# Kernel optimization log

Measured on AMD Instinct MI355X. Metric: run time of the kernel, lower is better.

The kernel has to match this reference:

```python
import jax, jax.numpy as jnp
import numpy as np

NUM_BINS = 10
NUM_CLASSES = 128
ALPHA = 0.999
LABEL_SMOOTHING = 0.0


def setup_inputs() -> dict:
    key = jax.random.key(0)
    k1, k2, k3 = jax.random.split(key, 3)
    B, T, C = 16, 4096, NUM_CLASSES
    return {
        "pred_logits": jax.random.normal(k1, (B, T, C), dtype=jnp.float32),
        "target_prob": jax.random.uniform(k2, (B, T, C), dtype=jnp.float32),
        "mask": jax.random.uniform(k3, (B, T, 1), dtype=jnp.float32),
        "GD_stat_ema": jnp.ones((NUM_BINS,), dtype=jnp.float32),
        "label_stat_ema_each_class": jnp.ones((NUM_CLASSES * 3,), dtype=jnp.float32),
    }


def _bce_with_logits(x, t):
    # numerically stable BCEWithLogitsLoss, reduction='none'
    return jnp.maximum(x, 0.0) - x * t + jnp.log1p(jnp.exp(-jnp.abs(x)))


def _update_ema(ema, hist, num_bins):
    hist = hist / jnp.maximum(hist.sum(), 1e-10) * num_bins
    ema = ema * ALPHA + (1.0 - ALPHA) * hist
    return ema / jnp.maximum(ema.sum(), 1e-10) * num_bins


def reference(pred_logits, target_prob, mask, GD_stat_ema, label_stat_ema_each_class):
    m = jnp.broadcast_to(mask, pred_logits.shape)
    tp = jnp.clip(target_prob, LABEL_SMOOTHING, 1.0 - LABEL_SMOOTHING)

    raw_loss = _bce_with_logits(pred_logits, tp)
    pred_prob = jax.nn.sigmoid(pred_logits)
    grad_mag = jnp.abs(pred_prob - tp)

    bin_idx = jnp.clip(jnp.floor(grad_mag * NUM_BINS).astype(jnp.int32), 0, NUM_BINS - 1)
    GD_weights = 1.0 / jax.lax.stop_gradient(GD_stat_ema[bin_idx])

    # per-class 3-way probability bin: idx in [0, 3*num_classes)
    tpi = jnp.clip(jnp.floor(tp * 3.0).astype(jnp.int32), 0, 2) + 3 * jnp.arange(NUM_CLASSES, dtype=jnp.int32)
    classes_weights = 1.0 / jax.lax.stop_gradient(label_stat_ema_each_class[tpi])

    weights = jnp.sqrt(GD_weights * classes_weights)
    loss = (raw_loss * weights * m).sum() / jnp.maximum(m.sum(), 1e-10)

    # weighted histograms (bincount with float weights)
    GD_hist = jnp.zeros((NUM_BINS,), dtype=jnp.float32).at[bin_idx.ravel()].add(m.ravel())
    label_hist = jnp.zeros((NUM_CLASSES * 3,), dtype=jnp.float32).at[tpi.ravel()].add(m.ravel())

    GD_ema_new = _update_ema(GD_stat_ema, GD_hist, NUM_BINS)
    label_ema_new = _update_ema(label_stat_ema_each_class, label_hist, NUM_CLASSES * 3)
    return loss, GD_ema_new, label_ema_new
```

## Files before the change

kernel.cpp:

```cpp
#include <hip/hip_runtime.h>

#define NBINS 10
#define LBINS 384
#define NOUT  395
#define PSTRIDE 400
#define PQ (PSTRIDE / 4)
#define BLOCK 256

typedef float f32x4 __attribute__((ext_vector_type(4)));

#define TO_LDS(p) ((__attribute__((address_space(3))) void*)(uintptr_t)(p))
#define TO_GLB(p) ((const __attribute__((address_space(1))) void*)(uintptr_t)(p))

#define SGRID 1024
#define SGSTR (SGRID * BLOCK)

__device__ __forceinline__ void ghm_elem4(
    const f32x4 xv, const f32x4 tv, const float m,
    const float wl[4][3], const float* s_rsgd,
    float lab[4][3], float gdl[NBINS], float& loss_acc)
{
    const float xs[4] = {xv.x, xv.y, xv.z, xv.w};
    const float ts[4] = {tv.x, tv.y, tv.z, tv.w};
    unsigned pack = 0u;
#pragma unroll
    for (int j = 0; j < 4; ++j) {
        const float x  = xs[j];
        const float tp = ts[j];
        const float E  = __expf(-fabsf(x));
        const float z  = 1.f + E;
        const float raw = fmaxf(x, 0.f) - x * tp + __logf(z);
        const float inv = __builtin_amdgcn_rcpf(z);
        const float tps = (x >= 0.f) ? tp : 1.f - tp;
        const float g   = fabsf(inv - tps);
        int bin = (int)(g * 10.f);  bin = bin > 9 ? 9 : bin;
        int t3  = (int)(tp * 3.f);  t3  = t3 > 2 ? 2 : t3;
        const float wlj = (t3 == 0) ? wl[j][0] : ((t3 == 1) ? wl[j][1] : wl[j][2]);
        const float w = s_rsgd[bin] * wlj;
        loss_acc = fmaf(raw * m, w, loss_acc);
#pragma unroll
        for (int t = 0; t < 3; ++t) lab[j][t] += (t3 == t) ? m : 0.f;
        pack += 1u << (3 * bin);
    }
#pragma unroll
    for (int b = 0; b < NBINS; ++b)
        gdl[b] = fmaf(m, (float)((pack >> (3 * b)) & 7u), gdl[b]);
}

__global__ __launch_bounds__(256) void ghm_main_l(
    const float* __restrict__ xg, const float* __restrict__ tg,
    const float* __restrict__ mask,
    const float* __restrict__ gd_ema, const float* __restrict__ lab_ema,
    float* __restrict__ ws)
{
    __shared__ float s_rsgd[NBINS];
    __shared__ float s_rslab[LBINS];
    __shared__ float s_out[PSTRIDE];
    __shared__ float s_red[4];
    __shared__ __align__(16) float s_pipe[4][8][2][256];

    const int tid = threadIdx.x;
    if (tid < NBINS) s_rsgd[tid] = __builtin_amdgcn_rsqf(gd_ema[tid]);
    for (int i = tid; i < LBINS; i += BLOCK) s_rslab[i] = __builtin_amdgcn_rsqf(lab_ema[i]);
    for (int i = tid; i < PSTRIDE; i += BLOCK) s_out[i] = 0.f;
    __syncthreads();

    const int c0 = (tid & 31) * 4;
    float wl[4][3];
#pragma unroll
    for (int j = 0; j < 4; ++j)
#pragma unroll
        for (int t = 0; t < 3; ++t) wl[j][t] = s_rslab[(c0 + j) * 3 + t];

    float lab[4][3] = {{0.f}};
    float gdl[NBINS];
#pragma unroll
    for (int b = 0; b < NBINS; ++b) gdl[b] = 0.f;
    float loss_acc = 0.f;

    const f32x4* x4 = (const f32x4*)xg;
    const f32x4* t4 = (const f32x4*)tg;
    const int lane = tid & 63, wv = tid >> 6;
    const int i0 = blockIdx.x * BLOCK + tid;

    float mv[8];
#pragma unroll
    for (int k = 0; k < 8; ++k) mv[k] = mask[(i0 + k * SGSTR) >> 5];
#pragma unroll
    for (int k = 0; k < 8; ++k) asm volatile("" : "+v"(mv[k]));

#pragma unroll
    for (int k = 0; k < 8; ++k) {
        const int i = i0 + k * SGSTR;
        __builtin_amdgcn_global_load_lds(TO_GLB(x4 + i), TO_LDS(&s_pipe[wv][k][0][0]), 16, 0, 0);
        __builtin_amdgcn_global_load_lds(TO_GLB(t4 + i), TO_LDS(&s_pipe[wv][k][1][0]), 16, 0, 0);
    }

#define GHM_STAGE(K, NW) do {                                                 \
        asm volatile("s_waitcnt vmcnt(" #NW ")" ::: "memory");                \
        const f32x4 xv = *(const f32x4*)&s_pipe[wv][K][0][lane * 4];          \
        const f32x4 tv = *(const f32x4*)&s_pipe[wv][K][1][lane * 4];          \
        ghm_elem4(xv, tv, mv[K], wl, s_rsgd, lab, gdl, loss_acc);             \
    } while (0)

    GHM_STAGE(0, 14); GHM_STAGE(1, 12); GHM_STAGE(2, 10); GHM_STAGE(3, 8);
    GHM_STAGE(4, 6);  GHM_STAGE(5, 4);  GHM_STAGE(6, 2);  GHM_STAGE(7, 0);
#undef GHM_STAGE

    float v = loss_acc;
#pragma unroll
    for (int off = 32; off > 0; off >>= 1) v += __shfl_down(v, off);
    if (lane == 0) s_red[wv] = v;
#pragma unroll
    for (int b = 0; b < NBINS; ++b) {
        float g = gdl[b];
#pragma unroll
        for (int off = 32; off > 0; off >>= 1) g += __shfl_down(g, off);
        if (lane == 0) atomicAdd(&s_out[1 + b], g);
    }
#pragma unroll
    for (int j = 0; j < 4; ++j)
#pragma unroll
        for (int t = 0; t < 3; ++t)
            atomicAdd(&s_out[11 + (c0 + j) * 3 + t], lab[j][t]);
    __syncthreads();

    float* slot = ws + (size_t)blockIdx.x * PSTRIDE;
    if (tid == 0) slot[0] = s_red[0] + s_red[1] + s_red[2] + s_red[3];
    if (tid >= 1) slot[tid] = s_out[tid];
    if (tid < PSTRIDE - BLOCK) slot[BLOCK + tid] = s_out[BLOCK + tid];
}

__global__ __launch_bounds__(256) void ghm_fin1(
    const float* __restrict__ ws, float* __restrict__ ws2, int nrows)
{
    __shared__ float4 r[BLOCK];
    const int tid = threadIdx.x;
    const float4* p = (const float4*)ws + blockIdx.x;
    float4 a = make_float4(0.f, 0.f, 0.f, 0.f);
    for (int b = tid; b < nrows; b += BLOCK) {
        float4 u = p[(size_t)b * PQ];
        a.x += u.x; a.y += u.y; a.z += u.z; a.w += u.w;
    }
    r[tid] = a;
    __syncthreads();
    for (int off = BLOCK / 2; off > 0; off >>= 1) {
        if (tid < off) {
            float4 u = r[tid + off];
            r[tid].x += u.x; r[tid].y += u.y; r[tid].z += u.z; r[tid].w += u.w;
        }
        __syncthreads();
    }
    if (tid == 0) ((float4*)ws2)[blockIdx.x] = r[0];
}

__global__ __launch_bounds__(512) void ghm_fin2(
    const float* __restrict__ sv_g,
    const float* __restrict__ gd_ema, const float* __restrict__ lab_ema,
    float* __restrict__ out)
{
    __shared__ float sv[PSTRIDE];
    __shared__ float red[512];
    __shared__ float s_sc[1];

    const int tid = threadIdx.x;
    if (tid < PSTRIDE) sv[tid] = sv_g[tid];
    __syncthreads();

    if (tid == 0) {
        float ms = 0.f;
        for (int b = 0; b < NBINS; ++b) ms += sv[1 + b];
        const float inv_m = 1.f / fmaxf(ms, 1e-10f);
        s_sc[0] = inv_m;
        out[0] = sv[0] * inv_m;
        float ge[NBINS], gs = 0.f;
        for (int b = 0; b < NBINS; ++b) {
            ge[b] = gd_ema[b] * 0.999f + 0.001f * (sv[1 + b] * inv_m * (float)NBINS);
            gs += ge[b];
        }
        const float ig = 1.f / fmaxf(gs, 1e-10f);
        for (int b = 0; b < NBINS; ++b) out[1 + b] = ge[b] * ig * (float)NBINS;
    }
    __syncthreads();
    const float inv_m = s_sc[0];

    float e = 0.f;
    if (tid < LBINS)
        e = lab_ema[tid] * 0.999f + 0.001f * (sv[11 + tid] * inv_m * (float)LBINS);
    red[tid] = e;
    __syncthreads();
    for (int off = 256; off > 0; off >>= 1) {
        if (tid < off) red[tid] += red[tid + off];
        __syncthreads();
    }
    const float ie = (float)LBINS / fmaxf(red[0], 1e-10f);
    if (tid < LBINS) out[11 + tid] = e * ie;
}

#define NSLICE 8
#define SLICE_STRIDE 512
#define AGRID 2048
#define AITER 4
#define AGSTR (AGRID * BLOCK)

__global__ __launch_bounds__(256) void ghm_main_a(
    const float* __restrict__ xg, const float* __restrict__ tg,
    const float* __restrict__ mask,
    const float* __restrict__ gd_ema, const float* __restrict__ lab_ema,
    float* __restrict__ ws)
{
    __shared__ float s_rsgd[NBINS];
    __shared__ float s_rslab[LBINS];
    __shared__ float s_hlab[LBINS];
    __shared__ float s_hgd[NBINS];
    __shared__ float s_red[4];

    const int tid = threadIdx.x;
    if (tid < NBINS) { s_rsgd[tid] = __builtin_amdgcn_rsqf(gd_ema[tid]); s_hgd[tid] = 0.f; }
    for (int i = tid; i < LBINS; i += BLOCK) {
        s_rslab[i] = __builtin_amdgcn_rsqf(lab_ema[i]);
        s_hlab[i]  = 0.f;
    }
    __syncthreads();

    const int c0 = (tid & 31) * 4;
    float wl[4][3];
#pragma unroll
    for (int j = 0; j < 4; ++j)
#pragma unroll
        for (int t = 0; t < 3; ++t) wl[j][t] = s_rslab[(c0 + j) * 3 + t];

    float lab[4][3] = {{0.f}};
    float gdl[NBINS];
#pragma unroll
    for (int b = 0; b < NBINS; ++b) gdl[b] = 0.f;
    float loss_acc = 0.f;

    const f32x4* x4 = (const f32x4*)xg;
    const f32x4* t4 = (const f32x4*)tg;
    const int i0 = blockIdx.x * BLOCK + tid;

    f32x4 xv[AITER], tv[AITER]; float mv[AITER];
#pragma unroll
    for (int k = 0; k < AITER; ++k) {
        const int i = i0 + k * AGSTR;
        xv[k] = x4[i]; tv[k] = t4[i]; mv[k] = mask[i >> 5];
    }
#pragma unroll
    for (int k = 0; k < AITER; ++k)
        ghm_elem4(xv[k], tv[k], mv[k], wl, s_rsgd, lab, gdl, loss_acc);

    const int lane = tid & 63, wv = tid >> 6;
    float v = loss_acc;
#pragma unroll
    for (int off = 32; off > 0; off >>= 1) v += __shfl_down(v, off);
    if (lane == 0) s_red[wv] = v;
#pragma unroll
    for (int b = 0; b < NBINS; ++b) {
        float g = gdl[b];
#pragma unroll
        for (int off = 32; off > 0; off >>= 1) g += __shfl_down(g, off);
        if (lane == 0) atomicAdd(&s_hgd[b], g);
    }
#pragma unroll
    for (int j = 0; j < 4; ++j)
#pragma unroll
        for (int t = 0; t < 3; ++t)
            atomicAdd(&s_hlab[(c0 + j) * 3 + t], lab[j][t]);
    __syncthreads();

    float* wss = ws + (blockIdx.x & (NSLICE - 1)) * SLICE_STRIDE;
    if (tid == 0) atomicAdd(&wss[0], s_red[0] + s_red[1] + s_red[2] + s_red[3]);
    if (tid < NBINS) atomicAdd(&wss[1 + tid], s_hgd[tid]);
    for (int e = tid; e < LBINS; e += BLOCK) atomicAdd(&wss[1 + NBINS + e], s_hlab[e]);
}

__global__ __launch_bounds__(512) void ghm_fin_a(
    const float* __restrict__ ws,
    const float* __restrict__ gd_ema, const float* __restrict__ lab_ema,
    float* __restrict__ out)
{
    __shared__ float red[512];
    __shared__ float s_gde[NBINS];
    __shared__ float s_gesum;

    const int tid = threadIdx.x;
    float v = 0.f;
    if (tid < NOUT) {
#pragma unroll
        for (int s = 0; s < NSLICE; ++s) v += ws[s * SLICE_STRIDE + tid];
    }
    red[tid] = (tid >= 1 && tid < 1 + NBINS) ? v : 0.f;
    __syncthreads();
    for (int off = 256; off > 0; off >>= 1) {
        if (tid < off) red[tid] += red[tid + off];
        __syncthreads();
    }
    const float msum = red[0];
    __syncthreads();
    const float inv_m = 1.f / fmaxf(msum, 1e-10f);
    if (tid == 0) out[0] = v * inv_m;
    if (tid >= 1 && tid < 1 + NBINS) {
        float hn = v * inv_m * (float)NBINS;
        s_gde[tid - 1] = gd_ema[tid - 1] * 0.999f + 0.001f * hn;
    }
    __syncthreads();
    if (tid == 0) {
        float s = 0.f;
        for (int b = 0; b < NBINS; ++b) s += s_gde[b];
        s_gesum = s;
    }
    __syncthreads();
    if (tid >= 1 && tid < 1 + NBINS)
        out[tid] = s_gde[tid - 1] / fmaxf(s_gesum, 1e-10f) * (float)NBINS;

    float e = 0.f;
    if (tid >= 1 + NBINS && tid < NOUT) {
        float hn = v * inv_m * (float)LBINS;
        e = lab_ema[tid - 1 - NBINS] * 0.999f + 0.001f * hn;
    }
    red[tid] = e;
    __syncthreads();
    for (int off = 256; off > 0; off >>= 1) {
        if (tid < off) red[tid] += red[tid + off];
        __syncthreads();
    }
    const float esum = red[0];
    if (tid >= 1 + NBINS && tid < NOUT)
        out[tid] = e / fmaxf(esum, 1e-10f) * (float)LBINS;
}

extern "C" void kernel_launch(void* const* d_in, const int* in_sizes, int n_in,
                              void* d_out, int out_size, void* d_ws, size_t ws_size,
                              hipStream_t stream)
{
    const float* logits  = (const float*)d_in[0];
    const float* tprob   = (const float*)d_in[1];
    const float* mask    = (const float*)d_in[2];
    const float* gd_ema  = (const float*)d_in[3];
    const float* lab_ema = (const float*)d_in[4];
    float* out = (float*)d_out;
    float* ws  = (float*)d_ws;

    const size_t need = ((size_t)SGRID * PSTRIDE + PSTRIDE) * sizeof(float);
    if (ws_size >= need) {
        float* ws2 = ws + (size_t)SGRID * PSTRIDE;
        ghm_main_l<<<SGRID, BLOCK, 0, stream>>>(logits, tprob, mask, gd_ema, lab_ema, ws);
        ghm_fin1<<<PQ, BLOCK, 0, stream>>>(ws, ws2, SGRID);
        ghm_fin2<<<1, 512, 0, stream>>>(ws2, gd_ema, lab_ema, out);
    } else {
        hipMemsetAsync(ws, 0, NSLICE * SLICE_STRIDE * sizeof(float), stream);
        ghm_main_a<<<AGRID, BLOCK, 0, stream>>>(logits, tprob, mask, gd_ema, lab_ema, ws);
        ghm_fin_a<<<1, 512, 0, stream>>>(ws, gd_ema, lab_ema, out);
    }
}
```

Before: 141.4 us.

## Replace LDS-staged async loads with register double-buffered direct loads

Result: slower. 153.5 us (+8.6%).

```diff
diff --git a/kernel.cpp b/kernel.cpp
--- a/kernel.cpp
+++ b/kernel.cpp
@@ -9,11 +9,9 @@
 
 typedef float f32x4 __attribute__((ext_vector_type(4)));
 
-#define TO_LDS(p) ((__attribute__((address_space(3))) void*)(uintptr_t)(p))
-#define TO_GLB(p) ((const __attribute__((address_space(1))) void*)(uintptr_t)(p))
-
-#define SGRID 1024
-#define SGSTR (SGRID * BLOCK)
+#define PGRID 2048
+#define PITER 4
+#define PGSTR (PGRID * BLOCK)
 
 __device__ __forceinline__ void ghm_elem4(
     const f32x4 xv, const f32x4 tv, const float m,
@@ -47,7 +45,7 @@
         gdl[b] = fmaf(m, (float)((pack >> (3 * b)) & 7u), gdl[b]);
 }
 
-__global__ __launch_bounds__(256) void ghm_main_l(
+__global__ __launch_bounds__(256) void ghm_main_p(
     const float* __restrict__ xg, const float* __restrict__ tg,
     const float* __restrict__ mask,
     const float* __restrict__ gd_ema, const float* __restrict__ lab_ema,
@@ -57,7 +55,6 @@
     __shared__ float s_rslab[LBINS];
     __shared__ float s_out[PSTRIDE];
     __shared__ float s_red[4];
-    __shared__ __align__(16) float s_pipe[4][8][2][256];
 
     const int tid = threadIdx.x;
     if (tid < NBINS) s_rsgd[tid] = __builtin_amdgcn_rsqf(gd_ema[tid]);
@@ -80,33 +77,25 @@
 
     const f32x4* x4 = (const f32x4*)xg;
     const f32x4* t4 = (const f32x4*)tg;
+    const int i0 = blockIdx.x * BLOCK + tid;
+
+    f32x4 xc = x4[i0], tc = t4[i0];
+    float mc = mask[i0 >> 5];
+    asm volatile("" : "+v"(xc), "+v"(tc), "+v"(mc));
+
+#pragma unroll
+    for (int k = 0; k < PITER; ++k) {
+        f32x4 xn, tn; float mn;
+        if (k + 1 < PITER) {
+            const int i = i0 + (k + 1) * PGSTR;
+            xn = x4[i]; tn = t4[i]; mn = mask[i >> 5];
+            asm volatile("" : "+v"(xn), "+v"(tn), "+v"(mn));
+        }
+        ghm_elem4(xc, tc, mc, wl, s_rsgd, lab, gdl, loss_acc);
+        if (k + 1 < PITER) { xc = xn; tc = tn; mc = mn; }
+    }
+
     const int lane = tid & 63, wv = tid >> 6;
-    const int i0 = blockIdx.x * BLOCK + tid;
-
-    float mv[8];
-#pragma unroll
-    for (int k = 0; k < 8; ++k) mv[k] = mask[(i0 + k * SGSTR) >> 5];
-#pragma unroll
-    for (int k = 0; k < 8; ++k) asm volatile("" : "+v"(mv[k]));
-
-#pragma unroll
-    for (int k = 0; k < 8; ++k) {
-        const int i = i0 + k * SGSTR;
-        __builtin_amdgcn_global_load_lds(TO_GLB(x4 + i), TO_LDS(&s_pipe[wv][k][0][0]), 16, 0, 0);
-        __builtin_amdgcn_global_load_lds(TO_GLB(t4 + i), TO_LDS(&s_pipe[wv][k][1][0]), 16, 0, 0);
-    }
-
-#define GHM_STAGE(K, NW) do {                                                 \
-        asm volatile("s_waitcnt vmcnt(" #NW ")" ::: "memory");                \
-        const f32x4 xv = *(const f32x4*)&s_pipe[wv][K][0][lane * 4];          \
-        const f32x4 tv = *(const f32x4*)&s_pipe[wv][K][1][lane * 4];          \
-        ghm_elem4(xv, tv, mv[K], wl, s_rsgd, lab, gdl, loss_acc);             \
-    } while (0)
-
-    GHM_STAGE(0, 14); GHM_STAGE(1, 12); GHM_STAGE(2, 10); GHM_STAGE(3, 8);
-    GHM_STAGE(4, 6);  GHM_STAGE(5, 4);  GHM_STAGE(6, 2);  GHM_STAGE(7, 0);
-#undef GHM_STAGE
-
     float v = loss_acc;
 #pragma unroll
     for (int off = 32; off > 0; off >>= 1) v += __shfl_down(v, off);
@@ -342,11 +331,11 @@
     float* out = (float*)d_out;
     float* ws  = (float*)d_ws;
 
-    const size_t need = ((size_t)SGRID * PSTRIDE + PSTRIDE) * sizeof(float);
+    const size_t need = ((size_t)PGRID * PSTRIDE + PSTRIDE) * sizeof(float);
     if (ws_size >= need) {
-        float* ws2 = ws + (size_t)SGRID * PSTRIDE;
-        ghm_main_l<<<SGRID, BLOCK, 0, stream>>>(logits, tprob, mask, gd_ema, lab_ema, ws);
-        ghm_fin1<<<PQ, BLOCK, 0, stream>>>(ws, ws2, SGRID);
+        float* ws2 = ws + (size_t)PGRID * PSTRIDE;
+        ghm_main_p<<<PGRID, BLOCK, 0, stream>>>(logits, tprob, mask, gd_ema, lab_ema, ws);
+        ghm_fin1<<<PQ, BLOCK, 0, stream>>>(ws, ws2, PGRID);
         ghm_fin2<<<1, 512, 0, stream>>>(ws2, gd_ema, lab_ema, out);
     } else {
         hipMemsetAsync(ws, 0, NSLICE * SLICE_STRIDE * sizeof(float), stream);
```
